# Kernel tuning notes

Hardware: AMD Instinct MI355X
Metric: run time of the kernel (lower is better)

The kernel has to match this reference:

```python
import jax, jax.numpy as jnp
import numpy as np

N = 100000          # nodes
E = 1600000         # edges
IN_DIM, HID, OUT = 64, 64, 32  # last GCN layer outputs OUT+1 channels


def setup_inputs() -> dict:
    key = jax.random.key(0)
    k0, k1, k2, k3 = jax.random.split(key, 4)
    x = jax.random.normal(k0, (N, IN_DIM), dtype=jnp.float32)
    edge_index = jax.random.randint(k1, (2, E), 0, N, dtype=jnp.int32)
    W1 = jax.random.normal(k2, (IN_DIM, HID), dtype=jnp.float32) / np.sqrt(IN_DIM)
    b1 = jnp.zeros((HID,), jnp.float32)
    W2 = jax.random.normal(k3, (HID, OUT + 1), dtype=jnp.float32) / np.sqrt(HID)
    b2 = jnp.zeros((OUT + 1,), jnp.float32)
    return {"x": x, "W1": W1, "b1": b1, "W2": W2, "b2": b2, "edge_index": edge_index}


def gcn_conv(x, src, dst, W, b):
    """PyG GCNConv: x' = D^{-1/2}(A+I)D^{-1/2} x W + b (self-loops added)."""
    n = x.shape[0]
    h = x @ W                                   # [N, F_out]
    # in-degree (over target nodes) + 1 for the self-loop
    deg = jnp.zeros((n,), x.dtype).at[dst].add(1.0) + 1.0
    dinv = jax.lax.rsqrt(deg)                   # [N]
    norm = dinv[src] * dinv[dst]                # [E]
    agg = jax.ops.segment_sum(h[src] * norm[:, None], dst, num_segments=n)
    agg = agg + h * (dinv * dinv)[:, None]      # self-loop contribution
    return agg + b


def reference(x, W1, b1, W2, b2, edge_index):
    src, dst = edge_index[0], edge_index[1]
    h = jax.nn.relu(gcn_conv(x, src, dst, W1, b1))
    # nn.Dropout(0.5) is identity in eval mode
    h = gcn_conv(h, src, dst, W2, b2)
    pos = h[:, :OUT]                            # [N, OUT]
    mass = jnp.exp(h[:, OUT:])                  # [N, 1]
    return pos, mass
```

## Files before the change

### kernel.cpp

```cpp
#include <hip/hip_runtime.h>
#include <hip/hip_bf16.h>


constexpr int NN = 100000;
constexpr int NE = 1600000;

constexpr int BSHIFT = 9;
constexpr int NBUCK = (NN + (1 << BSHIFT) - 1) >> BSHIFT;
constexpr int TILE = 4096;
constexpr int NTILE = (NE + TILE - 1) / TILE;
constexpr int CAP = 16384;


__device__ inline float bflo(unsigned w) { union { unsigned u; float f; } c; c.u = w << 16; return c.f; }
__device__ inline float bfhi(unsigned w) { union { unsigned u; float f; } c; c.u = w & 0xffff0000u; return c.f; }
__device__ inline unsigned f2bf_bits(float f) {
    __hip_bfloat16 h = __float2bfloat16(f);
    unsigned short u; __builtin_memcpy(&u, &h, 2); return (unsigned)u;
}
__device__ inline unsigned pack2(float a, float b) { return f2bf_bits(a) | (f2bf_bits(b) << 16); }


__global__ void k_zero(int* __restrict__ g) {
    int t = threadIdx.x;
    if (t < NBUCK) g[t] = 0;
}


__global__ __launch_bounds__(256) void k_split(const int* __restrict__ src,
                                               const int* __restrict__ dst,
                                               int* __restrict__ gcur,
                                               unsigned* __restrict__ pairs) {
    __shared__ int lcnt[256];
    __shared__ int lpre[256];
    __shared__ int gadj[NBUCK];
    __shared__ unsigned buf[TILE];
    __shared__ unsigned char bb[TILE];
    int tid = threadIdx.x;
    int base = blockIdx.x * TILE;

    lcnt[tid] = 0;
    __syncthreads();

    unsigned pk[16]; short bk[16]; short lp[16];
    #pragma unroll
    for (int k = 0; k < 16; ++k) {
        int e = base + k * 256 + tid;
        bk[k] = -1;
        if (e < NE) {
            int s = src[e], d = dst[e];
            int b = d >> BSHIFT;
            pk[k] = (unsigned)s | ((unsigned)(d & ((1 << BSHIFT) - 1)) << 17);
            bk[k] = (short)b;
            lp[k] = (short)atomicAdd(&lcnt[b], 1);
        }
    }
    __syncthreads();

    lpre[tid] = lcnt[tid];
    __syncthreads();
    for (int off = 1; off < 256; off <<= 1) {
        int v = (tid >= off) ? lpre[tid - off] : 0;
        __syncthreads();
        lpre[tid] += v;
        __syncthreads();
    }
    int total = lpre[255];

    if (tid < NBUCK) {
        int ex = lpre[tid] - lcnt[tid];
        gadj[tid] = tid * CAP + atomicAdd(&gcur[tid], lcnt[tid]) - ex;
    }
    __syncthreads();

    #pragma unroll
    for (int k = 0; k < 16; ++k) {
        if (bk[k] >= 0) {
            int b = bk[k];
            int i = (lpre[b] - lcnt[b]) + lp[k];
            buf[i] = pk[k];
            bb[i] = (unsigned char)b;
        }
    }
    __syncthreads();

    for (int i = tid; i < total; i += 256) {
        pairs[gadj[bb[i]] + i] = buf[i];
    }
}


__global__ __launch_bounds__(256) void k_bin2(const unsigned* __restrict__ pairs,
                                              const int* __restrict__ gcur,
                                              int* __restrict__ csr,
                                              int* __restrict__ rs,
                                              int* __restrict__ re,
                                              float* __restrict__ dinv) {
    int b = blockIdx.x;
    int lo = b << BSHIFT;
    int nn = min(1 << BSHIFT, NN - lo);
    int t = threadIdx.x;
    int beg = b * CAP;
    int endd = beg + gcur[b];

    __shared__ int lcnt[1 << BSHIFT];
    __shared__ int loff[1 << BSHIFT];
    __shared__ int wsum[256];

    for (int i = t; i < (1 << BSHIFT); i += 256) lcnt[i] = 0;
    __syncthreads();
    for (int idx = beg + t; idx < endd; idx += 256)
        atomicAdd(&lcnt[pairs[idx] >> 17], 1);
    __syncthreads();

    int v0 = lcnt[2 * t], v1 = lcnt[2 * t + 1];
    int s = v0 + v1;
    wsum[t] = s; __syncthreads();
    for (int off = 1; off < 256; off <<= 1) {
        int a = (t >= off) ? wsum[t - off] : 0;
        __syncthreads();
        wsum[t] += a;
        __syncthreads();
    }
    int ex = wsum[t] - s;
    loff[2 * t] = ex; loff[2 * t + 1] = ex + v0;
    __syncthreads();

    for (int i = t; i < nn; i += 256) {
        int st = beg + loff[i];
        rs[lo + i] = st;
        re[lo + i] = st + lcnt[i];
        dinv[lo + i] = rsqrtf((float)lcnt[i] + 1.0f);
    }
    __syncthreads();
    for (int i = t; i < (1 << BSHIFT); i += 256) lcnt[i] = 0;
    __syncthreads();

    for (int idx = beg + t; idx < endd; idx += 256) {
        unsigned v = pairs[idx];
        int dl = (int)(v >> 17);
        int p = atomicAdd(&lcnt[dl], 1);
        csr[beg + loff[dl] + p] = (int)(v & 0x1FFFFu);
    }
}


__global__ __launch_bounds__(256, 1) void k_gemm1(const float* __restrict__ x,
                                                  const float* __restrict__ W1,
                                                  const float* __restrict__ dinv,
                                                  unsigned short* __restrict__ ht1) {
    __shared__ float w[64 * 64];
    for (int t = threadIdx.x; t < 64 * 64; t += 256) w[t] = W1[t];
    __syncthreads();

    int i = blockIdx.x * 256 + threadIdx.x;
    if (i >= NN) return;

    float acc[64];
    #pragma unroll
    for (int f = 0; f < 64; ++f) acc[f] = 0.f;

    const float4* xp = reinterpret_cast<const float4*>(x + (size_t)i * 64);
    #pragma unroll
    for (int kc = 0; kc < 4; ++kc) {
        float4 c0 = xp[4 * kc + 0], c1 = xp[4 * kc + 1];
        float4 c2 = xp[4 * kc + 2], c3 = xp[4 * kc + 3];
        float xs[16] = {c0.x, c0.y, c0.z, c0.w, c1.x, c1.y, c1.z, c1.w,
                        c2.x, c2.y, c2.z, c2.w, c3.x, c3.y, c3.z, c3.w};
        #pragma unroll
        for (int kk = 0; kk < 16; ++kk) {
            float xk = xs[kk];
            const float4* wr = reinterpret_cast<const float4*>(w + (16 * kc + kk) * 64);
            #pragma unroll
            for (int f4 = 0; f4 < 16; ++f4) {
                float4 wv = wr[f4];
                acc[4 * f4 + 0] += xk * wv.x;
                acc[4 * f4 + 1] += xk * wv.y;
                acc[4 * f4 + 2] += xk * wv.z;
                acc[4 * f4 + 3] += xk * wv.w;
            }
        }
    }

    float di = dinv[i];
    uint4* hp = reinterpret_cast<uint4*>(ht1 + (size_t)i * 64);
    #pragma unroll
    for (int q = 0; q < 8; ++q) {
        uint4 v;
        v.x = pack2(acc[8 * q + 0] * di, acc[8 * q + 1] * di);
        v.y = pack2(acc[8 * q + 2] * di, acc[8 * q + 3] * di);
        v.z = pack2(acc[8 * q + 4] * di, acc[8 * q + 5] * di);
        v.w = pack2(acc[8 * q + 6] * di, acc[8 * q + 7] * di);
        hp[q] = v;
    }
}


__global__ __launch_bounds__(256) void k_gather1(const unsigned short* __restrict__ ht,
                                                 const int* __restrict__ rs,
                                                 const int* __restrict__ re,
                                                 const int* __restrict__ csr,
                                                 const float* __restrict__ dinv,
                                                 const float* __restrict__ b1,
                                                 const float* __restrict__ W2,
                                                 unsigned short* __restrict__ htp,
                                                 float* __restrict__ htm) {
    __shared__ float w2s[64 * 36];
    __shared__ float hs[32 * 68];

    for (int t = threadIdx.x; t < 64 * 36; t += 256) {
        int k = t / 36, c = t - k * 36;
        w2s[t] = (c < 33) ? W2[k * 33 + c] : 0.f;
    }

    int wid = (blockIdx.x * 256 + threadIdx.x) >> 3;
    int g = threadIdx.x >> 3;
    int l = threadIdx.x & 7;
    int beg = rs[wid], end = re[wid];

    float av[8];
    #pragma unroll
    for (int k = 0; k < 8; ++k) av[k] = 0.f;

    for (int j0 = beg; j0 < end; j0 += 8) {
        int jj = j0 + l;
        int sv = csr[min(jj, end - 1)];
        uint4 rows[8];
        #pragma unroll
        for (int e = 0; e < 8; ++e) {
            int s = __shfl(sv, e, 8);
            rows[e] = *reinterpret_cast<const uint4*>(ht + (size_t)s * 64 + 8 * l);
        }
        #pragma unroll
        for (int e = 0; e < 8; ++e) {
            float msk = (j0 + e < end) ? 1.f : 0.f;
            uint4 w = rows[e];
            av[0] += msk * bflo(w.x); av[1] += msk * bfhi(w.x);
            av[2] += msk * bflo(w.y); av[3] += msk * bfhi(w.y);
            av[4] += msk * bflo(w.z); av[5] += msk * bfhi(w.z);
            av[6] += msk * bflo(w.w); av[7] += msk * bfhi(w.w);
        }
    }

    uint4 sw = *reinterpret_cast<const uint4*>(ht + (size_t)wid * 64 + 8 * l);
    av[0] += bflo(sw.x); av[1] += bfhi(sw.x); av[2] += bflo(sw.y); av[3] += bfhi(sw.y);
    av[4] += bflo(sw.z); av[5] += bfhi(sw.z); av[6] += bflo(sw.w); av[7] += bfhi(sw.w);

    float di = dinv[wid];
    const float4* bp = reinterpret_cast<const float4*>(b1 + 8 * l);
    float4 bA = bp[0], bB = bp[1];
    float4 vA, vB;
    vA.x = fmaxf(di * av[0] + bA.x, 0.f); vA.y = fmaxf(di * av[1] + bA.y, 0.f);
    vA.z = fmaxf(di * av[2] + bA.z, 0.f); vA.w = fmaxf(di * av[3] + bA.w, 0.f);
    vB.x = fmaxf(di * av[4] + bB.x, 0.f); vB.y = fmaxf(di * av[5] + bB.y, 0.f);
    vB.z = fmaxf(di * av[6] + bB.z, 0.f); vB.w = fmaxf(di * av[7] + bB.w, 0.f);
    float* hp = hs + g * 68 + 8 * l;
    *reinterpret_cast<float4*>(hp)     = vA;
    *reinterpret_cast<float4*>(hp + 4) = vB;
    __syncthreads();

    float acc0 = 0.f, acc1 = 0.f, acc2 = 0.f, acc3 = 0.f, accm = 0.f;
    const float* hrow = hs + g * 68;
    #pragma unroll 8
    for (int k = 0; k < 64; ++k) {
        float hv = hrow[k];
        const float* wr = w2s + k * 36 + 4 * l;
        acc0 += hv * wr[0];
        acc1 += hv * wr[1];
        acc2 += hv * wr[2];
        acc3 += hv * wr[3];
        accm += hv * w2s[k * 36 + 32];
    }
    uint2 pv;
    pv.x = pack2(acc0 * di, acc1 * di);
    pv.y = pack2(acc2 * di, acc3 * di);
    *reinterpret_cast<uint2*>(htp + (size_t)wid * 32 + 4 * l) = pv;
    if (l == 0) htm[wid] = accm * di;
}


__global__ __launch_bounds__(256) void k_gather2(const unsigned short* __restrict__ htp,
                                                 const float* __restrict__ htm,
                                                 const int* __restrict__ rs,
                                                 const int* __restrict__ re,
                                                 const int* __restrict__ csr,
                                                 const float* __restrict__ dinv,
                                                 const float* __restrict__ b2,
                                                 float* __restrict__ out) {
    int wid = (blockIdx.x * 256 + threadIdx.x) >> 3;
    int l = threadIdx.x & 7;
    int beg = rs[wid], end = re[wid];

    float a0 = 0.f, a1 = 0.f, a2 = 0.f, a3 = 0.f, m = 0.f;
    for (int j0 = beg; j0 < end; j0 += 8) {
        int jj = j0 + l;
        int sv = csr[min(jj, end - 1)];
        if (jj < end) m += htm[sv];
        uint2 rows[8];
        #pragma unroll
        for (int e = 0; e < 8; ++e) {
            int s = __shfl(sv, e, 8);
            rows[e] = *reinterpret_cast<const uint2*>(htp + (size_t)s * 32 + 4 * l);
        }
        #pragma unroll
        for (int e = 0; e < 8; ++e) {
            float msk = (j0 + e < end) ? 1.f : 0.f;
            uint2 w = rows[e];
            a0 += msk * bflo(w.x); a1 += msk * bfhi(w.x);
            a2 += msk * bflo(w.y); a3 += msk * bfhi(w.y);
        }
    }

    m += __shfl_xor(m, 1); m += __shfl_xor(m, 2); m += __shfl_xor(m, 4);

    float di = dinv[wid];
    uint2 sw = *reinterpret_cast<const uint2*>(htp + (size_t)wid * 32 + 4 * l);
    a0 += bflo(sw.x); a1 += bfhi(sw.x); a2 += bflo(sw.y); a3 += bfhi(sw.y);
    const float4* bp = reinterpret_cast<const float4*>(b2 + 4 * l);
    float4 bv = bp[0];
    float4 v;
    v.x = di * a0 + bv.x; v.y = di * a1 + bv.y;
    v.z = di * a2 + bv.z; v.w = di * a3 + bv.w;
    *reinterpret_cast<float4*>(out + (size_t)wid * 32 + 4 * l) = v;
    if (l == 0) {
        out[(size_t)NN * 32 + wid] = expf(di * (m + htm[wid]) + b2[32]);
    }
}

extern "C" void kernel_launch(void* const* d_in, const int* in_sizes, int n_in,
                              void* d_out, int out_size, void* d_ws, size_t ws_size,
                              hipStream_t stream) {
    const float* x  = (const float*)d_in[0];
    const float* W1 = (const float*)d_in[1];
    const float* b1 = (const float*)d_in[2];
    const float* W2 = (const float*)d_in[3];
    const float* b2 = (const float*)d_in[4];
    const int*   ei = (const int*)d_in[5];
    const int* src = ei;
    const int* dst = ei + NE;
    float* out = (float*)d_out;

    char* p = (char*)d_ws;
    int* gcur   = (int*)p;              p += sizeof(int) * NBUCK;
    p = (char*)(((uintptr_t)p + 255) & ~(uintptr_t)255);
    int* rs     = (int*)p;              p += sizeof(int) * NN;
    p = (char*)(((uintptr_t)p + 255) & ~(uintptr_t)255);
    int* re     = (int*)p;              p += sizeof(int) * NN;
    p = (char*)(((uintptr_t)p + 255) & ~(uintptr_t)255);
    int* csr    = (int*)p;              p += sizeof(int) * (size_t)NBUCK * CAP;
    p = (char*)(((uintptr_t)p + 255) & ~(uintptr_t)255);
    unsigned* pairs = (unsigned*)p;     p += sizeof(unsigned) * (size_t)NBUCK * CAP;
    p = (char*)(((uintptr_t)p + 255) & ~(uintptr_t)255);
    float* dinv = (float*)p;            p += sizeof(float) * NN;
    p = (char*)(((uintptr_t)p + 255) & ~(uintptr_t)255);
    unsigned short* ht1 = (unsigned short*)p; p += sizeof(unsigned short) * (size_t)NN * 64;
    p = (char*)(((uintptr_t)p + 255) & ~(uintptr_t)255);
    unsigned short* htp = (unsigned short*)p; p += sizeof(unsigned short) * (size_t)NN * 32;
    p = (char*)(((uintptr_t)p + 255) & ~(uintptr_t)255);
    float* htm  = (float*)p;            p += sizeof(float) * NN;

    k_zero<<<1, 256, 0, stream>>>(gcur);
    k_split<<<NTILE, 256, 0, stream>>>(src, dst, gcur, pairs);
    k_bin2<<<NBUCK, 256, 0, stream>>>(pairs, gcur, csr, rs, re, dinv);

    k_gemm1<<<(NN + 255) / 256, 256, 0, stream>>>(x, W1, dinv, ht1);

    k_gather1<<<(NN * 8) / 256, 256, 0, stream>>>(ht1, rs, re, csr, dinv, b1, W2, htp, htm);

    k_gather2<<<(NN * 8) / 256, 256, 0, stream>>>(htp, htm, rs, re, csr, dinv, b2, out);
}
```

Before: 148.2 us.

## Sort nodes by in-degree to balance gather workloads across wavefronts

Builds a degree histogram in the CSR binning kernel, then scans it and computes a permutation of node ids ordered by in-degree. Both gather kernels use this permutation so that the 8-lane groups in a wavefront handle nodes of similar degree, which reduces divergence from uneven loop trip counts. The gathers also read each neighbour index straight from csr instead of broadcasting it with a shuffle. This costs two extra small kernels, one more indirection per node, and output writes that are scattered rather than sequential.

```diff
diff --git a/kernel.cpp b/kernel.cpp
--- a/kernel.cpp
+++ b/kernel.cpp
@@ -22,8 +22,8 @@
 
 
 __global__ void k_zero(int* __restrict__ g) {
-    int t = threadIdx.x;
-    if (t < NBUCK) g[t] = 0;
+    int t = blockIdx.x * blockDim.x + threadIdx.x;
+    if (t < NBUCK + 256) g[t] = 0;
 }
 
 
@@ -95,7 +95,8 @@
                                               int* __restrict__ csr,
                                               int* __restrict__ rs,
                                               int* __restrict__ re,
-                                              float* __restrict__ dinv) {
+                                              float* __restrict__ dinv,
+                                              int* __restrict__ deghist) {
     int b = blockIdx.x;
     int lo = b << BSHIFT;
     int nn = min(1 << BSHIFT, NN - lo);
@@ -106,8 +107,10 @@
     __shared__ int lcnt[1 << BSHIFT];
     __shared__ int loff[1 << BSHIFT];
     __shared__ int wsum[256];
+    __shared__ int hsh[256];
 
     for (int i = t; i < (1 << BSHIFT); i += 256) lcnt[i] = 0;
+    hsh[t] = 0;
     __syncthreads();
     for (int idx = beg + t; idx < endd; idx += 256)
         atomicAdd(&lcnt[pairs[idx] >> 17], 1);
@@ -131,7 +134,10 @@
         rs[lo + i] = st;
         re[lo + i] = st + lcnt[i];
         dinv[lo + i] = rsqrtf((float)lcnt[i] + 1.0f);
-    }
+        atomicAdd(&hsh[min(lcnt[i], 255)], 1);
+    }
+    __syncthreads();
+    if (hsh[t]) atomicAdd(&deghist[t], hsh[t]);
     __syncthreads();
     for (int i = t; i < (1 << BSHIFT); i += 256) lcnt[i] = 0;
     __syncthreads();
@@ -142,6 +148,41 @@
         int p = atomicAdd(&lcnt[dl], 1);
         csr[beg + loff[dl] + p] = (int)(v & 0x1FFFFu);
     }
+}
+
+
+__global__ void k_degscan(const int* __restrict__ deghist, int* __restrict__ degcur) {
+    __shared__ int sh[256];
+    int t = threadIdx.x;
+    int v = deghist[t];
+    sh[t] = v; __syncthreads();
+    for (int off = 1; off < 256; off <<= 1) {
+        int a = (t >= off) ? sh[t - off] : 0;
+        __syncthreads();
+        sh[t] += a;
+        __syncthreads();
+    }
+    degcur[t] = sh[t] - v;
+}
+
+
+__global__ __launch_bounds__(256) void k_place(const int* __restrict__ rs,
+                                               const int* __restrict__ re,
+                                               int* __restrict__ degcur,
+                                               int* __restrict__ perm) {
+    __shared__ int lh[256];
+    __shared__ int lb[256];
+    int t = threadIdx.x;
+    lh[t] = 0;
+    __syncthreads();
+    int i = blockIdx.x * 256 + t;
+    int deg = 0, lp = 0;
+    bool act = (i < NN);
+    if (act) { deg = min(re[i] - rs[i], 255); lp = atomicAdd(&lh[deg], 1); }
+    __syncthreads();
+    if (lh[t]) lb[t] = atomicAdd(&degcur[t], lh[t]);
+    __syncthreads();
+    if (act) perm[lb[deg] + lp] = i;
 }
 
 
@@ -200,6 +241,7 @@
                                                  const int* __restrict__ rs,
                                                  const int* __restrict__ re,
                                                  const int* __restrict__ csr,
+                                                 const int* __restrict__ perm,
                                                  const float* __restrict__ dinv,
                                                  const float* __restrict__ b1,
                                                  const float* __restrict__ W2,
@@ -213,7 +255,7 @@
         w2s[t] = (c < 33) ? W2[k * 33 + c] : 0.f;
     }
 
-    int wid = (blockIdx.x * 256 + threadIdx.x) >> 3;
+    int wid = perm[(blockIdx.x * 256 + threadIdx.x) >> 3];
     int g = threadIdx.x >> 3;
     int l = threadIdx.x & 7;
     int beg = rs[wid], end = re[wid];
@@ -223,12 +265,10 @@
     for (int k = 0; k < 8; ++k) av[k] = 0.f;
 
     for (int j0 = beg; j0 < end; j0 += 8) {
-        int jj = j0 + l;
-        int sv = csr[min(jj, end - 1)];
         uint4 rows[8];
         #pragma unroll
         for (int e = 0; e < 8; ++e) {
-            int s = __shfl(sv, e, 8);
+            int s = csr[min(j0 + e, end - 1)];
             rows[e] = *reinterpret_cast<const uint4*>(ht + (size_t)s * 64 + 8 * l);
         }
         #pragma unroll
@@ -284,22 +324,23 @@
                                                  const int* __restrict__ rs,
                                                  const int* __restrict__ re,
                                                  const int* __restrict__ csr,
+                                                 const int* __restrict__ perm,
                                                  const float* __restrict__ dinv,
                                                  const float* __restrict__ b2,
                                                  float* __restrict__ out) {
-    int wid = (blockIdx.x * 256 + threadIdx.x) >> 3;
+    int wid = perm[(blockIdx.x * 256 + threadIdx.x) >> 3];
     int l = threadIdx.x & 7;
     int beg = rs[wid], end = re[wid];
 
     float a0 = 0.f, a1 = 0.f, a2 = 0.f, a3 = 0.f, m = 0.f;
     for (int j0 = beg; j0 < end; j0 += 8) {
         int jj = j0 + l;
-        int sv = csr[min(jj, end - 1)];
-        if (jj < end) m += htm[sv];
+        int sown = csr[min(jj, end - 1)];
+        if (jj < end) m += htm[sown];
         uint2 rows[8];
         #pragma unroll
         for (int e = 0; e < 8; ++e) {
-            int s = __shfl(sv, e, 8);
+            int s = csr[min(j0 + e, end - 1)];
             rows[e] = *reinterpret_cast<const uint2*>(htp + (size_t)s * 32 + 4 * l);
         }
         #pragma unroll
@@ -341,7 +382,12 @@
     float* out = (float*)d_out;
 
     char* p = (char*)d_ws;
-    int* gcur   = (int*)p;              p += sizeof(int) * NBUCK;
+    int* gcur    = (int*)p;             p += sizeof(int) * NBUCK;
+    int* deghist = (int*)p;             p += sizeof(int) * 256;
+    p = (char*)(((uintptr_t)p + 255) & ~(uintptr_t)255);
+    int* degcur  = (int*)p;             p += sizeof(int) * 256;
+    p = (char*)(((uintptr_t)p + 255) & ~(uintptr_t)255);
+    int* perm    = (int*)p;             p += sizeof(int) * NN;
     p = (char*)(((uintptr_t)p + 255) & ~(uintptr_t)255);
     int* rs     = (int*)p;              p += sizeof(int) * NN;
     p = (char*)(((uintptr_t)p + 255) & ~(uintptr_t)255);
@@ -359,13 +405,16 @@
     p = (char*)(((uintptr_t)p + 255) & ~(uintptr_t)255);
     float* htm  = (float*)p;            p += sizeof(float) * NN;
 
-    k_zero<<<1, 256, 0, stream>>>(gcur);
+    k_zero<<<2, 256, 0, stream>>>(gcur);
     k_split<<<NTILE, 256, 0, stream>>>(src, dst, gcur, pairs);
-    k_bin2<<<NBUCK, 256, 0, stream>>>(pairs, gcur, csr, rs, re, dinv);
+    k_bin2<<<NBUCK, 256, 0, stream>>>(pairs, gcur, csr, rs, re, dinv, deghist);
+
+    k_degscan<<<1, 256, 0, stream>>>(deghist, degcur);
+    k_place<<<(NN + 255) / 256, 256, 0, stream>>>(rs, re, degcur, perm);
 
     k_gemm1<<<(NN + 255) / 256, 256, 0, stream>>>(x, W1, dinv, ht1);
 
-    k_gather1<<<(NN * 8) / 256, 256, 0, stream>>>(ht1, rs, re, csr, dinv, b1, W2, htp, htm);
-
-    k_gather2<<<(NN * 8) / 256, 256, 0, stream>>>(htp, htm, rs, re, csr, dinv, b2, out);
-}
+    k_gather1<<<(NN * 8) / 256, 256, 0, stream>>>(ht1, rs, re, csr, perm, dinv, b1, W2, htp, htm);
+
+    k_gather2<<<(NN * 8) / 256, 256, 0, stream>>>(htp, htm, rs, re, csr, perm, dinv, b2, out);
+}
```

Result: slower. 167.7 us (+13.2%).

## Merge edge-splitting and first GEMM into one launch, apply source dinv in gather

Applied to the files above, without the earlier changes.

The first-layer GEMM no longer depends on the degree normalization. It now runs as extra blocks of the edge-bucketing kernel, so the two independent stages share one launch and can overlap. The per-source dinv scaling moves into the first gather, which loads dinv[src] per edge and broadcasts it with shuffles. This removes one kernel launch and the serial dependency of the GEMM on bucketing. The costs are extra per-edge dinv loads in the gather, and shared memory and register pressure, since both roles share one kernel with launch bounds of one block.

```diff
diff --git a/kernel.cpp b/kernel.cpp
--- a/kernel.cpp
+++ b/kernel.cpp
@@ -9,6 +9,7 @@
 constexpr int NBUCK = (NN + (1 << BSHIFT) - 1) >> BSHIFT;
 constexpr int TILE = 4096;
 constexpr int NTILE = (NE + TILE - 1) / TILE;
+constexpr int GEMM1CH = (NN + 255) / 256;
 constexpr int CAP = 16384;
 
 
@@ -27,65 +28,116 @@
 }
 
 
-__global__ __launch_bounds__(256) void k_split(const int* __restrict__ src,
-                                               const int* __restrict__ dst,
-                                               int* __restrict__ gcur,
-                                               unsigned* __restrict__ pairs) {
-    __shared__ int lcnt[256];
-    __shared__ int lpre[256];
-    __shared__ int gadj[NBUCK];
-    __shared__ unsigned buf[TILE];
-    __shared__ unsigned char bb[TILE];
+__global__ __launch_bounds__(256, 1) void k_split_gemm(const int* __restrict__ src,
+                                                       const int* __restrict__ dst,
+                                                       int* __restrict__ gcur,
+                                                       unsigned* __restrict__ pairs,
+                                                       const float* __restrict__ x,
+                                                       const float* __restrict__ W1,
+                                                       unsigned short* __restrict__ ht1) {
+    __shared__ __align__(16) char smem[23552];
     int tid = threadIdx.x;
-    int base = blockIdx.x * TILE;
-
-    lcnt[tid] = 0;
-    __syncthreads();
-
-    unsigned pk[16]; short bk[16]; short lp[16];
-    #pragma unroll
-    for (int k = 0; k < 16; ++k) {
-        int e = base + k * 256 + tid;
-        bk[k] = -1;
-        if (e < NE) {
-            int s = src[e], d = dst[e];
-            int b = d >> BSHIFT;
-            pk[k] = (unsigned)s | ((unsigned)(d & ((1 << BSHIFT) - 1)) << 17);
-            bk[k] = (short)b;
-            lp[k] = (short)atomicAdd(&lcnt[b], 1);
-        }
-    }
-    __syncthreads();
-
-    lpre[tid] = lcnt[tid];
-    __syncthreads();
-    for (int off = 1; off < 256; off <<= 1) {
-        int v = (tid >= off) ? lpre[tid - off] : 0;
-        __syncthreads();
-        lpre[tid] += v;
-        __syncthreads();
-    }
-    int total = lpre[255];
-
-    if (tid < NBUCK) {
-        int ex = lpre[tid] - lcnt[tid];
-        gadj[tid] = tid * CAP + atomicAdd(&gcur[tid], lcnt[tid]) - ex;
-    }
-    __syncthreads();
-
-    #pragma unroll
-    for (int k = 0; k < 16; ++k) {
-        if (bk[k] >= 0) {
-            int b = bk[k];
-            int i = (lpre[b] - lcnt[b]) + lp[k];
-            buf[i] = pk[k];
-            bb[i] = (unsigned char)b;
-        }
-    }
-    __syncthreads();
-
-    for (int i = tid; i < total; i += 256) {
-        pairs[gadj[bb[i]] + i] = buf[i];
+
+    if (blockIdx.x < NTILE) {
+        int* lcnt = (int*)smem;
+        int* lpre = lcnt + 256;
+        int* gadj = lpre + 256;
+        unsigned* buf = (unsigned*)(gadj + 200);
+        unsigned char* bb = (unsigned char*)(buf + TILE);
+        int base = blockIdx.x * TILE;
+
+        lcnt[tid] = 0;
+        __syncthreads();
+
+        unsigned pk[16]; short bk[16]; short lp[16];
+        #pragma unroll
+        for (int k = 0; k < 16; ++k) {
+            int e = base + k * 256 + tid;
+            bk[k] = -1;
+            if (e < NE) {
+                int s = src[e], d = dst[e];
+                int b = d >> BSHIFT;
+                pk[k] = (unsigned)s | ((unsigned)(d & ((1 << BSHIFT) - 1)) << 17);
+                bk[k] = (short)b;
+                lp[k] = (short)atomicAdd(&lcnt[b], 1);
+            }
+        }
+        __syncthreads();
+
+        lpre[tid] = lcnt[tid];
+        __syncthreads();
+        for (int off = 1; off < 256; off <<= 1) {
+            int v = (tid >= off) ? lpre[tid - off] : 0;
+            __syncthreads();
+            lpre[tid] += v;
+            __syncthreads();
+        }
+        int total = lpre[255];
+
+        if (tid < NBUCK) {
+            int ex = lpre[tid] - lcnt[tid];
+            gadj[tid] = tid * CAP + atomicAdd(&gcur[tid], lcnt[tid]) - ex;
+        }
+        __syncthreads();
+
+        #pragma unroll
+        for (int k = 0; k < 16; ++k) {
+            if (bk[k] >= 0) {
+                int b = bk[k];
+                int i = (lpre[b] - lcnt[b]) + lp[k];
+                buf[i] = pk[k];
+                bb[i] = (unsigned char)b;
+            }
+        }
+        __syncthreads();
+
+        for (int i = tid; i < total; i += 256) {
+            pairs[gadj[bb[i]] + i] = buf[i];
+        }
+    } else {
+        float* w = (float*)smem;
+        for (int t = tid; t < 64 * 64; t += 256) w[t] = W1[t];
+        __syncthreads();
+
+        int i = (blockIdx.x - NTILE) * 256 + tid;
+        if (i >= NN) return;
+
+        float acc[64];
+        #pragma unroll
+        for (int f = 0; f < 64; ++f) acc[f] = 0.f;
+
+        const float4* xp = reinterpret_cast<const float4*>(x + (size_t)i * 64);
+        #pragma unroll
+        for (int kc = 0; kc < 4; ++kc) {
+            float4 c0 = xp[4 * kc + 0], c1 = xp[4 * kc + 1];
+            float4 c2 = xp[4 * kc + 2], c3 = xp[4 * kc + 3];
+            float xs[16] = {c0.x, c0.y, c0.z, c0.w, c1.x, c1.y, c1.z, c1.w,
+                            c2.x, c2.y, c2.z, c2.w, c3.x, c3.y, c3.z, c3.w};
+            #pragma unroll
+            for (int kk = 0; kk < 16; ++kk) {
+                float xk = xs[kk];
+                const float4* wr = reinterpret_cast<const float4*>(w + (16 * kc + kk) * 64);
+                #pragma unroll
+                for (int f4 = 0; f4 < 16; ++f4) {
+                    float4 wv = wr[f4];
+                    acc[4 * f4 + 0] += xk * wv.x;
+                    acc[4 * f4 + 1] += xk * wv.y;
+                    acc[4 * f4 + 2] += xk * wv.z;
+                    acc[4 * f4 + 3] += xk * wv.w;
+                }
+            }
+        }
+
+        uint4* hp = reinterpret_cast<uint4*>(ht1 + (size_t)i * 64);
+        #pragma unroll
+        for (int q = 0; q < 8; ++q) {
+            uint4 v;
+            v.x = pack2(acc[8 * q + 0], acc[8 * q + 1]);
+            v.y = pack2(acc[8 * q + 2], acc[8 * q + 3]);
+            v.z = pack2(acc[8 * q + 4], acc[8 * q + 5]);
+            v.w = pack2(acc[8 * q + 6], acc[8 * q + 7]);
+            hp[q] = v;
+        }
     }
 }
 
@@ -145,57 +197,6 @@
 }
 
 
-__global__ __launch_bounds__(256, 1) void k_gemm1(const float* __restrict__ x,
-                                                  const float* __restrict__ W1,
-                                                  const float* __restrict__ dinv,
-                                                  unsigned short* __restrict__ ht1) {
-    __shared__ float w[64 * 64];
-    for (int t = threadIdx.x; t < 64 * 64; t += 256) w[t] = W1[t];
-    __syncthreads();
-
-    int i = blockIdx.x * 256 + threadIdx.x;
-    if (i >= NN) return;
-
-    float acc[64];
-    #pragma unroll
-    for (int f = 0; f < 64; ++f) acc[f] = 0.f;
-
-    const float4* xp = reinterpret_cast<const float4*>(x + (size_t)i * 64);
-    #pragma unroll
-    for (int kc = 0; kc < 4; ++kc) {
-        float4 c0 = xp[4 * kc + 0], c1 = xp[4 * kc + 1];
-        float4 c2 = xp[4 * kc + 2], c3 = xp[4 * kc + 3];
-        float xs[16] = {c0.x, c0.y, c0.z, c0.w, c1.x, c1.y, c1.z, c1.w,
-                        c2.x, c2.y, c2.z, c2.w, c3.x, c3.y, c3.z, c3.w};
-        #pragma unroll
-        for (int kk = 0; kk < 16; ++kk) {
-            float xk = xs[kk];
-            const float4* wr = reinterpret_cast<const float4*>(w + (16 * kc + kk) * 64);
-            #pragma unroll
-            for (int f4 = 0; f4 < 16; ++f4) {
-                float4 wv = wr[f4];
-                acc[4 * f4 + 0] += xk * wv.x;
-                acc[4 * f4 + 1] += xk * wv.y;
-                acc[4 * f4 + 2] += xk * wv.z;
-                acc[4 * f4 + 3] += xk * wv.w;
-            }
-        }
-    }
-
-    float di = dinv[i];
-    uint4* hp = reinterpret_cast<uint4*>(ht1 + (size_t)i * 64);
-    #pragma unroll
-    for (int q = 0; q < 8; ++q) {
-        uint4 v;
-        v.x = pack2(acc[8 * q + 0] * di, acc[8 * q + 1] * di);
-        v.y = pack2(acc[8 * q + 2] * di, acc[8 * q + 3] * di);
-        v.z = pack2(acc[8 * q + 4] * di, acc[8 * q + 5] * di);
-        v.w = pack2(acc[8 * q + 6] * di, acc[8 * q + 7] * di);
-        hp[q] = v;
-    }
-}
-
-
 __global__ __launch_bounds__(256) void k_gather1(const unsigned short* __restrict__ ht,
                                                  const int* __restrict__ rs,
                                                  const int* __restrict__ re,
@@ -225,15 +226,17 @@
     for (int j0 = beg; j0 < end; j0 += 8) {
         int jj = j0 + l;
         int sv = csr[min(jj, end - 1)];
-        uint4 rows[8];
+        float dvl = dinv[sv];
+        uint4 rows[8]; float ds[8];
         #pragma unroll
         for (int e = 0; e < 8; ++e) {
             int s = __shfl(sv, e, 8);
+            ds[e] = __shfl(dvl, e, 8);
             rows[e] = *reinterpret_cast<const uint4*>(ht + (size_t)s * 64 + 8 * l);
         }
         #pragma unroll
         for (int e = 0; e < 8; ++e) {
-            float msk = (j0 + e < end) ? 1.f : 0.f;
+            float msk = (j0 + e < end) ? ds[e] : 0.f;
             uint4 w = rows[e];
             av[0] += msk * bflo(w.x); av[1] += msk * bfhi(w.x);
             av[2] += msk * bflo(w.y); av[3] += msk * bfhi(w.y);
@@ -242,11 +245,13 @@
         }
     }
 
+    float di = dinv[wid];
     uint4 sw = *reinterpret_cast<const uint4*>(ht + (size_t)wid * 64 + 8 * l);
-    av[0] += bflo(sw.x); av[1] += bfhi(sw.x); av[2] += bflo(sw.y); av[3] += bfhi(sw.y);
-    av[4] += bflo(sw.z); av[5] += bfhi(sw.z); av[6] += bflo(sw.w); av[7] += bfhi(sw.w);
-
-    float di = dinv[wid];
+    av[0] += di * bflo(sw.x); av[1] += di * bfhi(sw.x);
+    av[2] += di * bflo(sw.y); av[3] += di * bfhi(sw.y);
+    av[4] += di * bflo(sw.z); av[5] += di * bfhi(sw.z);
+    av[6] += di * bflo(sw.w); av[7] += di * bfhi(sw.w);
+
     const float4* bp = reinterpret_cast<const float4*>(b1 + 8 * l);
     float4 bA = bp[0], bB = bp[1];
     float4 vA, vB;
@@ -360,11 +365,9 @@
     float* htm  = (float*)p;            p += sizeof(float) * NN;
 
     k_zero<<<1, 256, 0, stream>>>(gcur);
-    k_split<<<NTILE, 256, 0, stream>>>(src, dst, gcur, pairs);
+    k_split_gemm<<<NTILE + GEMM1CH, 256, 0, stream>>>(src, dst, gcur, pairs, x, W1, ht1);
     k_bin2<<<NBUCK, 256, 0, stream>>>(pairs, gcur, csr, rs, re, dinv);
 
-    k_gemm1<<<(NN + 255) / 256, 256, 0, stream>>>(x, W1, dinv, ht1);
-
     k_gather1<<<(NN * 8) / 256, 256, 0, stream>>>(ht1, rs, re, csr, dinv, b1, W2, htp, htm);
 
     k_gather2<<<(NN * 8) / 256, 256, 0, stream>>>(htp, htm, rs, re, csr, dinv, b2, out);
```

After: 145.9 us, median of 2. No clear change (-1.5%).
